# Performance work log

Measured on AMD Instinct MI355X. Metric: run time of the kernel, lower is better.

Reference implementation:

```python
import jax, jax.numpy as jnp
import numpy as np

D_MODEL = 1024
N_HEADS = 16
D_HEAD = D_MODEL // N_HEADS
LN_EPS = 1e-5


def setup_inputs() -> dict:
    key = jax.random.key(0)
    ks = jax.random.split(key, 8)
    B, T = 4, 2048
    s = 1.0 / np.sqrt(D_MODEL)
    return {
        "encoder_seq": jax.random.normal(ks[0], (B, T, D_MODEL), jnp.float32),
        "decoder_seq": jax.random.normal(ks[1], (B, T, D_MODEL), jnp.float32),
        "Wq": jax.random.normal(ks[2], (D_MODEL, D_MODEL), jnp.float32) * s,
        "bq": jnp.zeros((D_MODEL,), jnp.float32),
        "Wk": jax.random.normal(ks[3], (D_MODEL, D_MODEL), jnp.float32) * s,
        "bk": jnp.zeros((D_MODEL,), jnp.float32),
        "Wv": jax.random.normal(ks[4], (D_MODEL, D_MODEL), jnp.float32) * s,
        "bv": jnp.zeros((D_MODEL,), jnp.float32),
        "ln_gamma": jnp.ones((D_MODEL,), jnp.float32),
        "ln_beta": jnp.zeros((D_MODEL,), jnp.float32),
    }


def layer_norm(x, gamma, beta):
    mu = jnp.mean(x, axis=-1, keepdims=True)
    var = jnp.mean(jnp.square(x - mu), axis=-1, keepdims=True)
    return (x - mu) * jax.lax.rsqrt(var + LN_EPS) * gamma + beta


def reference(encoder_seq, decoder_seq, Wq, bq, Wk, bk, Wv, bv, ln_gamma, ln_beta):
    B, T_dec, _ = decoder_seq.shape
    T_enc = encoder_seq.shape[1]
    # projections (torch Linear: x @ W^T + b)
    q = (decoder_seq @ Wq.T + bq).reshape(B, T_dec, N_HEADS, D_HEAD)
    k = (encoder_seq @ Wk.T + bk).reshape(B, T_enc, N_HEADS, D_HEAD)
    v = (encoder_seq @ Wv.T + bv).reshape(B, T_enc, N_HEADS, D_HEAD)
    scale = 1.0 / np.sqrt(D_HEAD)
    # softmax-free attention: scale*(Q K^T) V == scale * Q (K^T V); avoid [T_dec,T_enc]
    kv = jnp.einsum("bthd,bthe->bhde", k, v)          # [B,H,dh,dh]
    att = jnp.einsum("bqhd,bhde->bqhe", q, kv) * scale  # [B,T_dec,H,dh]
    att = att.reshape(B, T_dec, D_MODEL)
    # dropout is identity in eval mode; residual + LayerNorm
    return layer_norm(att + decoder_seq, ln_gamma, ln_beta)
```

## Files before the change

kernel.cpp:

```cpp
#include <hip/hip_runtime.h>
#include <hip/hip_bf16.h>
#include <stdint.h>
#include <stddef.h>

typedef __attribute__((ext_vector_type(8))) __bf16 bf16x8;
typedef __attribute__((ext_vector_type(4))) float f32x4;

#define DMODEL 1024
#define HEADS  16
#define BATCH  4
#define TSEQ   2048
#define MROWS  (BATCH * TSEQ)
#define NE     (MROWS * DMODEL)
#define NW     (DMODEL * DMODEL)

#define MiB (size_t)1048576
#define QB_OFF   ((size_t)0)
#define KB_OFF   (16 * MiB)
#define VB_OFF   (32 * MiB)
#define ENC_OFF  (48 * MiB)
#define KVP_OFF  (48 * MiB)
#define DEC_OFF  (64 * MiB)
#define WB_OFF   (80 * MiB)
#define KVT_OFF  (86 * MiB)

__global__ __launch_bounds__(256)
void conv_all(const float* __restrict__ enc, const float* __restrict__ dec,
              const float* __restrict__ Wq, const float* __restrict__ Wk,
              const float* __restrict__ Wv,
              __bf16* __restrict__ encB, __bf16* __restrict__ decB,
              __bf16* __restrict__ WB)
{
    const int i = (blockIdx.x * 256 + threadIdx.x) * 8;
    const float* src;
    __bf16* dst;
    int off;
    if (i < NE)            { src = enc; dst = encB; off = i; }
    else if (i < 2 * NE)   { src = dec; dst = decB; off = i - NE; }
    else {
        const int j = i - 2 * NE;
        const int sel = j >> 20;
        off = j & (NW - 1);
        src = (sel == 0) ? Wq : (sel == 1) ? Wk : Wv;
        dst = WB + (size_t)sel * NW;
    }
    f32x4 a = *(const f32x4*)(src + off);
    f32x4 b = *(const f32x4*)(src + off + 4);
    bf16x8 o;
#pragma unroll
    for (int j = 0; j < 4; ++j) { o[j] = (__bf16)a[j]; o[j + 4] = (__bf16)b[j]; }
    *(bf16x8*)(dst + off) = o;
}

__device__ __forceinline__ bf16x8 frag(const __bf16* reg, int rowl, int kh, int g4)
{
    const int slot = ((kh << 2) + g4) ^ (rowl & 7);
    return *(const bf16x8*)(reg + rowl * 64 + slot * 8);
}

__device__ __forceinline__ void stage_half(const __bf16* gbase, int kt,
                                           __bf16* reg, int tid)
{
#pragma unroll
    for (int p = 0; p < 2; ++p) {
        const int c = tid + p * 512;
        const int row = c >> 3, slot = c & 7;
        const __bf16* src = gbase + (size_t)row * DMODEL + kt * 64
                            + ((slot ^ (row & 7)) << 3);
        __builtin_amdgcn_global_load_lds(
            (const __attribute__((address_space(1))) void*)src,
            (__attribute__((address_space(3))) void*)(reg + c * 8), 16, 0, 0);
    }
}

#define VMW(N)  asm volatile("s_waitcnt vmcnt(" #N ")" ::: "memory")
#define LGKM0() asm volatile("s_waitcnt lgkmcnt(0)" ::: "memory")

#define KPHASE(PAR, STAGE_CODE, WAIT_CODE)                                    \
  {                                                                           \
    bf16x8 af[4][2], bfv[4][2];                                               \
    _Pragma("unroll") for (int mf = 0; mf < 4; ++mf)                          \
      _Pragma("unroll") for (int kh = 0; kh < 2; ++kh)                        \
        af[mf][kh] = frag(&ldsA[(PAR) * 8192], wm * 64 + mf * 16 + l4, kh, g4); \
    _Pragma("unroll") for (int nf = 0; nf < 4; ++nf)                          \
      _Pragma("unroll") for (int kh = 0; kh < 2; ++kh)                        \
        bfv[nf][kh] = frag(&ldsB[(PAR) * 16384 + bh2 * 8192],                 \
                           (wn & 1) * 64 + nf * 16 + l4, kh, g4);             \
    LGKM0();                                                                  \
    __builtin_amdgcn_sched_barrier(0);                                        \
    __builtin_amdgcn_s_barrier();                                             \
    STAGE_CODE;                                                               \
    __builtin_amdgcn_sched_barrier(0);                                        \
    __builtin_amdgcn_s_setprio(1);                                            \
    _Pragma("unroll") for (int mf = 0; mf < 4; ++mf)                          \
      _Pragma("unroll") for (int nf = 0; nf < 4; ++nf)                        \
        _Pragma("unroll") for (int kh = 0; kh < 2; ++kh)                      \
          acc[mf][nf] = __builtin_amdgcn_mfma_f32_16x16x32_bf16(              \
              af[mf][kh], bfv[nf][kh], acc[mf][nf], 0, 0, 0);                 \
    __builtin_amdgcn_s_setprio(0);                                            \
    WAIT_CODE;                                                                \
    __builtin_amdgcn_s_barrier();                                             \
  }

__global__ __launch_bounds__(512, 2)
void qkv_gemm(const __bf16* __restrict__ decB, const __bf16* __restrict__ encB,
              const __bf16* __restrict__ WB,
              const float* __restrict__ bq, const float* __restrict__ bk,
              const float* __restrict__ bv,
              __bf16* __restrict__ Qb, __bf16* __restrict__ Kb,
              __bf16* __restrict__ Vb)
{
    __shared__ __align__(16) __bf16 ldsA[2 * 8192];
    __shared__ __align__(16) __bf16 ldsB[2 * 16384];

    const int tid  = threadIdx.x;
    const int lane = tid & 63;
    const int wv   = tid >> 6;
    const int wm   = wv >> 2;
    const int wn   = wv & 3;
    const int bh2  = wn >> 1;
    const int l4   = lane & 15;
    const int g4   = lane >> 4;

    const int bid  = blockIdx.x;
    const int slab = bid & 7;
    const int idx  = bid >> 3;
    const int r    = idx >> 3;
    const int sel  = r >> 2;
    const int bn   = r & 3;
    const int bm   = slab * 8 + (idx & 7);

    const __bf16* A    = (sel == 0) ? decB : encB;
    const __bf16* Wb   = WB + (size_t)sel * NW + (size_t)(bn * 256) * DMODEL;
    const float*  bias = (sel == 0) ? bq : (sel == 1) ? bk : bv;
    __bf16*       C    = (sel == 0) ? Qb : (sel == 1) ? Kb : Vb;

    const __bf16* Ab = A + (size_t)(bm * 128) * DMODEL;

    auto stage_tile = [&](int par, int kt) {
        stage_half(Ab,                        kt, ldsA + par * 8192,         tid);
        stage_half(Wb,                        kt, ldsB + par * 16384,        tid);
        stage_half(Wb + (size_t)128 * DMODEL, kt, ldsB + par * 16384 + 8192, tid);
    };

    f32x4 acc[4][4] = {};

    stage_tile(0, 0);
    stage_tile(1, 1);
    VMW(6);
    __builtin_amdgcn_sched_barrier(0);
    __builtin_amdgcn_s_barrier();

    for (int i = 0; i < 8; ++i) {
        KPHASE(0, { if (i < 7) stage_tile(0, 2 * i + 2); },
                  { if (i < 7) { VMW(6); } else { VMW(0); } })
        KPHASE(1, { if (i < 7) stage_tile(1, 2 * i + 3); },
                  { if (i < 7) { VMW(6); } else { VMW(0); } })
    }

#pragma unroll
    for (int mf = 0; mf < 4; ++mf)
#pragma unroll
        for (int nf = 0; nf < 4; ++nf) {
            const int gm0 = bm * 128 + wm * 64 + mf * 16 + g4 * 4;
            const int gn  = bn * 256 + wn * 64 + nf * 16 + l4;
            const float bv2 = bias[gn];
#pragma unroll
            for (int j = 0; j < 4; ++j)
                C[(size_t)(gm0 + j) * DMODEL + gn] =
                    (__bf16)(acc[mf][nf][j] + bv2);
        }
}

__global__ __launch_bounds__(256)
void kv_mm(const __bf16* __restrict__ Kb, const __bf16* __restrict__ Vb,
           float* __restrict__ kvp)
{
    __shared__ __align__(16) float Ks[128][64];
    __shared__ __align__(16) float Vs[128][64];

    const int tid = threadIdx.x;
    const int bh  = blockIdx.x;
    const int ch  = blockIdx.y;
    const int b   = bh >> 4, h = bh & 15;
    const int w   = tid >> 6, lane = tid & 63;
    const int dg  = (lane >> 3) * 8;
    const int eg  = (lane & 7) * 8;
    const size_t base = (size_t)b * TSEQ + (size_t)ch * 512;

    f32x4 acc[8][2] = {};

    for (int ss = 0; ss < 4; ++ss) {
        __syncthreads();
#pragma unroll
        for (int i = 0; i < 4; ++i) {
            const int e = i * 2048 + tid * 8;
            const int t = e >> 6, d = e & 63;
            bf16x8 k8 = *(const bf16x8*)&Kb[(base + ss * 128 + t) * DMODEL + h * 64 + d];
            bf16x8 v8 = *(const bf16x8*)&Vb[(base + ss * 128 + t) * DMODEL + h * 64 + d];
            f32x4 kf0, kf1, vf0, vf1;
#pragma unroll
            for (int j = 0; j < 4; ++j) {
                kf0[j] = (float)k8[j]; kf1[j] = (float)k8[j + 4];
                vf0[j] = (float)v8[j]; vf1[j] = (float)v8[j + 4];
            }
            *(f32x4*)&Ks[t][d]     = kf0;
            *(f32x4*)&Ks[t][d + 4] = kf1;
            *(f32x4*)&Vs[t][d]     = vf0;
            *(f32x4*)&Vs[t][d + 4] = vf1;
        }
        __syncthreads();

#pragma unroll 4
        for (int tt = 0; tt < 32; ++tt) {
            const int t = w * 32 + tt;
            f32x4 kd0 = *(const f32x4*)&Ks[t][dg];
            f32x4 kd1 = *(const f32x4*)&Ks[t][dg + 4];
            f32x4 ve0 = *(const f32x4*)&Vs[t][eg];
            f32x4 ve1 = *(const f32x4*)&Vs[t][eg + 4];
#pragma unroll
            for (int rr = 0; rr < 8; ++rr) {
                const float kd = (rr < 4) ? kd0[rr] : kd1[rr - 4];
                acc[rr][0] += ve0 * kd;
                acc[rr][1] += ve1 * kd;
            }
        }
    }

    float* red = &Ks[0][0];
    __syncthreads();
    if (w >= 2) {
        float* dstw = red + (w - 2) * 4096 + dg * 64 + eg;
#pragma unroll
        for (int rr = 0; rr < 8; ++rr) {
            *(f32x4*)(dstw + rr * 64)     = acc[rr][0];
            *(f32x4*)(dstw + rr * 64 + 4) = acc[rr][1];
        }
    }
    __syncthreads();
    if (w < 2) {
        const float* srcw = red + w * 4096 + dg * 64 + eg;
#pragma unroll
        for (int rr = 0; rr < 8; ++rr) {
            acc[rr][0] += *(const f32x4*)(srcw + rr * 64);
            acc[rr][1] += *(const f32x4*)(srcw + rr * 64 + 4);
        }
    }
    __syncthreads();
    if (w == 1) {
        float* dstw = red + dg * 64 + eg;
#pragma unroll
        for (int rr = 0; rr < 8; ++rr) {
            *(f32x4*)(dstw + rr * 64)     = acc[rr][0];
            *(f32x4*)(dstw + rr * 64 + 4) = acc[rr][1];
        }
    }
    __syncthreads();
    if (w == 0) {
        const float* srcw = red + dg * 64 + eg;
        float* o = kvp + ((size_t)ch * 64 + bh) * 4096 + (size_t)dg * 64 + eg;
#pragma unroll
        for (int rr = 0; rr < 8; ++rr) {
            f32x4 s0 = acc[rr][0] + *(const f32x4*)(srcw + rr * 64);
            f32x4 s1 = acc[rr][1] + *(const f32x4*)(srcw + rr * 64 + 4);
            *(f32x4*)(o + rr * 64)     = s0;
            *(f32x4*)(o + rr * 64 + 4) = s1;
        }
    }
}

__global__ __launch_bounds__(256)
void kv_reduce(const float* __restrict__ kvp, __bf16* __restrict__ kvT)
{
    const int idx = blockIdx.x * 256 + threadIdx.x;
    const int bh  = idx >> 12;
    const int rem = idx & 4095;
    const int d = rem >> 6, e = rem & 63;
    float s = 0.f;
#pragma unroll
    for (int c = 0; c < 4; ++c) s += kvp[((size_t)c * 64 + bh) * 4096 + rem];
    kvT[(size_t)bh * 4096 + e * 64 + d] = (__bf16)(s * 0.125f);
}

__global__ __launch_bounds__(256)
void att_ln(const __bf16* __restrict__ Q, const __bf16* __restrict__ kvT,
            const __bf16* __restrict__ decB, const float* __restrict__ gamma,
            const float* __restrict__ beta, float* __restrict__ out)
{
    __shared__ __align__(16) __bf16 att_s[32][1032];

    const int tid  = threadIdx.x;
    const int lane = tid & 63;
    const int w    = tid >> 6;
    const int l4   = lane & 15, g4 = lane >> 4;
    const int t0   = blockIdx.x * 32;
    const int b    = t0 >> 11;

#pragma unroll
    for (int i = 0; i < 4; ++i) {
        const int h = w * 4 + i;
        f32x4 acc[2][4] = {};
#pragma unroll
        for (int kk = 0; kk < 2; ++kk) {
            bf16x8 a0 = *(const bf16x8*)&Q[(size_t)(t0 + l4) * DMODEL + h * 64 + kk * 32 + g4 * 8];
            bf16x8 a1 = *(const bf16x8*)&Q[(size_t)(t0 + 16 + l4) * DMODEL + h * 64 + kk * 32 + g4 * 8];
#pragma unroll
            for (int n = 0; n < 4; ++n) {
                bf16x8 bb = *(const bf16x8*)&kvT[(size_t)(b * 16 + h) * 4096 + (n * 16 + l4) * 64 + kk * 32 + g4 * 8];
                acc[0][n] = __builtin_amdgcn_mfma_f32_16x16x32_bf16(a0, bb, acc[0][n], 0, 0, 0);
                acc[1][n] = __builtin_amdgcn_mfma_f32_16x16x32_bf16(a1, bb, acc[1][n], 0, 0, 0);
            }
        }
#pragma unroll
        for (int m = 0; m < 2; ++m)
#pragma unroll
            for (int n = 0; n < 4; ++n)
#pragma unroll
                for (int j = 0; j < 4; ++j)
                    att_s[m * 16 + g4 * 4 + j][h * 64 + n * 16 + l4] = (__bf16)acc[m][n][j];
    }
    __syncthreads();

    const int rr = tid >> 3, seg = tid & 7;
    const size_t grow = (size_t)t0 + rr;
    float sum = 0.f, ss2 = 0.f;
#pragma unroll
    for (int i = 0; i < 16; ++i) {
        const int c0 = seg * 8 + i * 64;
        bf16x8 av = *(const bf16x8*)&att_s[rr][c0];
        bf16x8 dv = *(const bf16x8*)&decB[grow * DMODEL + c0];
        bf16x8 xs;
#pragma unroll
        for (int j = 0; j < 8; ++j) {
            const float x = (float)av[j] + (float)dv[j];
            sum += x; ss2 += x * x;
            xs[j] = (__bf16)x;
        }
        *(bf16x8*)&att_s[rr][c0] = xs;
    }
    sum += __shfl_xor(sum, 1); ss2 += __shfl_xor(ss2, 1);
    sum += __shfl_xor(sum, 2); ss2 += __shfl_xor(ss2, 2);
    sum += __shfl_xor(sum, 4); ss2 += __shfl_xor(ss2, 4);
    const float mu   = sum * (1.f / 1024.f);
    const float var  = ss2 * (1.f / 1024.f) - mu * mu;
    const float rstd = rsqrtf(var + 1e-5f);

#pragma unroll
    for (int i = 0; i < 16; ++i) {
        const int c0 = seg * 8 + i * 64;
        bf16x8 xv = *(const bf16x8*)&att_s[rr][c0];
        f32x4 g0 = *(const f32x4*)&gamma[c0];
        f32x4 g1 = *(const f32x4*)&gamma[c0 + 4];
        f32x4 b0 = *(const f32x4*)&beta[c0];
        f32x4 b1 = *(const f32x4*)&beta[c0 + 4];
        f32x4 y0, y1;
#pragma unroll
        for (int j = 0; j < 4; ++j) {
            y0[j] = ((float)xv[j]     - mu) * rstd * g0[j] + b0[j];
            y1[j] = ((float)xv[j + 4] - mu) * rstd * g1[j] + b1[j];
        }
        *(f32x4*)&out[grow * DMODEL + c0]     = y0;
        *(f32x4*)&out[grow * DMODEL + c0 + 4] = y1;
    }
}

extern "C" void kernel_launch(void* const* d_in, const int* in_sizes, int n_in,
                              void* d_out, int out_size, void* d_ws, size_t ws_size,
                              hipStream_t stream)
{
    const float* enc   = (const float*)d_in[0];
    const float* dec   = (const float*)d_in[1];
    const float* Wq    = (const float*)d_in[2];
    const float* bq    = (const float*)d_in[3];
    const float* Wk    = (const float*)d_in[4];
    const float* bk    = (const float*)d_in[5];
    const float* Wv    = (const float*)d_in[6];
    const float* bv    = (const float*)d_in[7];
    const float* gamma = (const float*)d_in[8];
    const float* beta  = (const float*)d_in[9];

    char* ws = (char*)d_ws;
    __bf16* Qb   = (__bf16*)(ws + QB_OFF);
    __bf16* Kb   = (__bf16*)(ws + KB_OFF);
    __bf16* Vb   = (__bf16*)(ws + VB_OFF);
    __bf16* encB = (__bf16*)(ws + ENC_OFF);
    float*  kvp  = (float*) (ws + KVP_OFF);
    __bf16* decB = (__bf16*)(ws + DEC_OFF);
    __bf16* WB   = (__bf16*)(ws + WB_OFF);
    __bf16* kvT  = (__bf16*)(ws + KVT_OFF);

    conv_all<<<9728, 256, 0, stream>>>(enc, dec, Wq, Wk, Wv, encB, decB, WB);
    qkv_gemm<<<768, 512, 0, stream>>>(decB, encB, WB, bq, bk, bv, Qb, Kb, Vb);
    kv_mm<<<dim3(64, 4), 256, 0, stream>>>(Kb, Vb, kvp);
    kv_reduce<<<1024, 256, 0, stream>>>(kvp, kvT);
    att_ln<<<256, 256, 0, stream>>>(Qb, kvT, decB, gamma, beta, (float*)d_out);
}
```

Before: 123.4 us.

## Fuse activation fp32-to-bf16 conversion into GEMM staging, drop activation pre-conversion

```diff
diff --git a/kernel.cpp b/kernel.cpp
--- a/kernel.cpp
+++ b/kernel.cpp
@@ -18,48 +18,61 @@
 #define QB_OFF   ((size_t)0)
 #define KB_OFF   (16 * MiB)
 #define VB_OFF   (32 * MiB)
-#define ENC_OFF  (48 * MiB)
 #define KVP_OFF  (48 * MiB)
-#define DEC_OFF  (64 * MiB)
-#define WB_OFF   (80 * MiB)
-#define KVT_OFF  (86 * MiB)
+#define WB_OFF   (52 * MiB)
+#define KVT_OFF  (58 * MiB)
 
 __global__ __launch_bounds__(256)
-void conv_all(const float* __restrict__ enc, const float* __restrict__ dec,
-              const float* __restrict__ Wq, const float* __restrict__ Wk,
-              const float* __restrict__ Wv,
-              __bf16* __restrict__ encB, __bf16* __restrict__ decB,
-              __bf16* __restrict__ WB)
-{
-    const int i = (blockIdx.x * 256 + threadIdx.x) * 8;
-    const float* src;
-    __bf16* dst;
-    int off;
-    if (i < NE)            { src = enc; dst = encB; off = i; }
-    else if (i < 2 * NE)   { src = dec; dst = decB; off = i - NE; }
-    else {
-        const int j = i - 2 * NE;
-        const int sel = j >> 20;
-        off = j & (NW - 1);
-        src = (sel == 0) ? Wq : (sel == 1) ? Wk : Wv;
-        dst = WB + (size_t)sel * NW;
-    }
-    f32x4 a = *(const f32x4*)(src + off);
-    f32x4 b = *(const f32x4*)(src + off + 4);
+void conv_w(const float* __restrict__ Wq, const float* __restrict__ Wk,
+            const float* __restrict__ Wv, __bf16* __restrict__ WB)
+{
+    const int bid = blockIdx.x;
+    const int sel = bid >> 9, blk = bid & 511;
+    const float* src = (sel == 0) ? Wq : (sel == 1) ? Wk : Wv;
+    const int i = blk * 2048 + threadIdx.x * 8;
+    f32x4 a = *(const f32x4*)(src + i);
+    f32x4 b = *(const f32x4*)(src + i + 4);
     bf16x8 o;
 #pragma unroll
     for (int j = 0; j < 4; ++j) { o[j] = (__bf16)a[j]; o[j + 4] = (__bf16)b[j]; }
-    *(bf16x8*)(dst + off) = o;
-}
-
-__device__ __forceinline__ bf16x8 frag(const __bf16* reg, int rowl, int kh, int g4)
+    *(bf16x8*)&WB[(size_t)sel * NW + i] = o;
+}
+
+__device__ __forceinline__ bf16x8 fragB(const __bf16* reg, int rowl, int kh, int g4)
 {
     const int slot = ((kh << 2) + g4) ^ (rowl & 7);
     return *(const bf16x8*)(reg + rowl * 64 + slot * 8);
 }
 
-__device__ __forceinline__ void stage_half(const __bf16* gbase, int kt,
-                                           __bf16* reg, int tid)
+__device__ __forceinline__ bf16x8 fragA32(const float* buf, int rowl, int kh, int g4)
+{
+    const int s0 = kh * 8 + g4 * 2;
+    const float* base = buf + rowl * 64;
+    f32x4 a = *(const f32x4*)(base + ((s0 ^ (rowl & 15)) << 2));
+    f32x4 b = *(const f32x4*)(base + (((s0 + 1) ^ (rowl & 15)) << 2));
+    bf16x8 o;
+#pragma unroll
+    for (int j = 0; j < 4; ++j) { o[j] = (__bf16)a[j]; o[j + 4] = (__bf16)b[j]; }
+    return o;
+}
+
+__device__ __forceinline__ void stageA32(const float* gbase, int kt,
+                                         float* reg, int tid)
+{
+#pragma unroll
+    for (int p = 0; p < 4; ++p) {
+        const int c = tid + p * 512;
+        const int row = c >> 4, slot = c & 15;
+        const float* src = gbase + (size_t)row * DMODEL + kt * 64
+                           + ((slot ^ (row & 15)) << 2);
+        __builtin_amdgcn_global_load_lds(
+            (const __attribute__((address_space(1))) void*)src,
+            (__attribute__((address_space(3))) void*)(reg + c * 4), 16, 0, 0);
+    }
+}
+
+__device__ __forceinline__ void stage_halfB(const __bf16* gbase, int kt,
+                                            __bf16* reg, int tid)
 {
 #pragma unroll
     for (int p = 0; p < 2; ++p) {
@@ -81,11 +94,11 @@
     bf16x8 af[4][2], bfv[4][2];                                               \
     _Pragma("unroll") for (int mf = 0; mf < 4; ++mf)                          \
       _Pragma("unroll") for (int kh = 0; kh < 2; ++kh)                        \
-        af[mf][kh] = frag(&ldsA[(PAR) * 8192], wm * 64 + mf * 16 + l4, kh, g4); \
+        af[mf][kh] = fragA32(&ldsAf[(PAR) * 8192], wm * 64 + mf * 16 + l4, kh, g4); \
     _Pragma("unroll") for (int nf = 0; nf < 4; ++nf)                          \
       _Pragma("unroll") for (int kh = 0; kh < 2; ++kh)                        \
-        bfv[nf][kh] = frag(&ldsB[(PAR) * 16384 + bh2 * 8192],                 \
-                           (wn & 1) * 64 + nf * 16 + l4, kh, g4);             \
+        bfv[nf][kh] = fragB(&ldsB[(PAR) * 16384 + bh2 * 8192],                \
+                            (wn & 1) * 64 + nf * 16 + l4, kh, g4);            \
     LGKM0();                                                                  \
     __builtin_amdgcn_sched_barrier(0);                                        \
     __builtin_amdgcn_s_barrier();                                             \
@@ -103,14 +116,14 @@
   }
 
 __global__ __launch_bounds__(512, 2)
-void qkv_gemm(const __bf16* __restrict__ decB, const __bf16* __restrict__ encB,
+void qkv_gemm(const float* __restrict__ dec, const float* __restrict__ enc,
               const __bf16* __restrict__ WB,
               const float* __restrict__ bq, const float* __restrict__ bk,
               const float* __restrict__ bv,
               __bf16* __restrict__ Qb, __bf16* __restrict__ Kb,
               __bf16* __restrict__ Vb)
 {
-    __shared__ __align__(16) __bf16 ldsA[2 * 8192];
+    __shared__ __align__(16) float  ldsAf[2 * 8192];
     __shared__ __align__(16) __bf16 ldsB[2 * 16384];
 
     const int tid  = threadIdx.x;
@@ -130,32 +143,32 @@
     const int bn   = r & 3;
     const int bm   = slab * 8 + (idx & 7);
 
-    const __bf16* A    = (sel == 0) ? decB : encB;
+    const float*  A    = (sel == 0) ? dec : enc;
     const __bf16* Wb   = WB + (size_t)sel * NW + (size_t)(bn * 256) * DMODEL;
     const float*  bias = (sel == 0) ? bq : (sel == 1) ? bk : bv;
     __bf16*       C    = (sel == 0) ? Qb : (sel == 1) ? Kb : Vb;
 
-    const __bf16* Ab = A + (size_t)(bm * 128) * DMODEL;
+    const float* Ab = A + (size_t)(bm * 128) * DMODEL;
 
     auto stage_tile = [&](int par, int kt) {
-        stage_half(Ab,                        kt, ldsA + par * 8192,         tid);
-        stage_half(Wb,                        kt, ldsB + par * 16384,        tid);
-        stage_half(Wb + (size_t)128 * DMODEL, kt, ldsB + par * 16384 + 8192, tid);
+        stageA32(Ab, kt, ldsAf + par * 8192, tid);
+        stage_halfB(Wb,                        kt, ldsB + par * 16384,        tid);
+        stage_halfB(Wb + (size_t)128 * DMODEL, kt, ldsB + par * 16384 + 8192, tid);
     };
 
     f32x4 acc[4][4] = {};
 
     stage_tile(0, 0);
     stage_tile(1, 1);
-    VMW(6);
+    VMW(8);
     __builtin_amdgcn_sched_barrier(0);
     __builtin_amdgcn_s_barrier();
 
     for (int i = 0; i < 8; ++i) {
         KPHASE(0, { if (i < 7) stage_tile(0, 2 * i + 2); },
-                  { if (i < 7) { VMW(6); } else { VMW(0); } })
+                  { if (i < 7) { VMW(8); } else { VMW(0); } })
         KPHASE(1, { if (i < 7) stage_tile(1, 2 * i + 3); },
-                  { if (i < 7) { VMW(6); } else { VMW(0); } })
+                  { if (i < 7) { VMW(8); } else { VMW(0); } })
     }
 
 #pragma unroll
@@ -284,7 +297,7 @@
 
 __global__ __launch_bounds__(256)
 void att_ln(const __bf16* __restrict__ Q, const __bf16* __restrict__ kvT,
-            const __bf16* __restrict__ decB, const float* __restrict__ gamma,
+            const float* __restrict__ dec, const float* __restrict__ gamma,
             const float* __restrict__ beta, float* __restrict__ out)
 {
     __shared__ __align__(16) __bf16 att_s[32][1032];
@@ -328,13 +341,15 @@
     for (int i = 0; i < 16; ++i) {
         const int c0 = seg * 8 + i * 64;
         bf16x8 av = *(const bf16x8*)&att_s[rr][c0];
-        bf16x8 dv = *(const bf16x8*)&decB[grow * DMODEL + c0];
+        f32x4 d0 = *(const f32x4*)&dec[grow * DMODEL + c0];
+        f32x4 d1 = *(const f32x4*)&dec[grow * DMODEL + c0 + 4];
         bf16x8 xs;
 #pragma unroll
-        for (int j = 0; j < 8; ++j) {
-            const float x = (float)av[j] + (float)dv[j];
-            sum += x; ss2 += x * x;
-            xs[j] = (__bf16)x;
+        for (int j = 0; j < 4; ++j) {
+            const float x0 = (float)av[j] + d0[j];
+            const float x1 = (float)av[j + 4] + d1[j];
+            sum += x0 + x1; ss2 += x0 * x0 + x1 * x1;
+            xs[j] = (__bf16)x0; xs[j + 4] = (__bf16)x1;
         }
         *(bf16x8*)&att_s[rr][c0] = xs;
     }
@@ -380,18 +395,16 @@
     const float* beta  = (const float*)d_in[9];
 
     char* ws = (char*)d_ws;
-    __bf16* Qb   = (__bf16*)(ws + QB_OFF);
-    __bf16* Kb   = (__bf16*)(ws + KB_OFF);
-    __bf16* Vb   = (__bf16*)(ws + VB_OFF);
-    __bf16* encB = (__bf16*)(ws + ENC_OFF);
-    float*  kvp  = (float*) (ws + KVP_OFF);
-    __bf16* decB = (__bf16*)(ws + DEC_OFF);
-    __bf16* WB   = (__bf16*)(ws + WB_OFF);
-    __bf16* kvT  = (__bf16*)(ws + KVT_OFF);
-
-    conv_all<<<9728, 256, 0, stream>>>(enc, dec, Wq, Wk, Wv, encB, decB, WB);
-    qkv_gemm<<<768, 512, 0, stream>>>(decB, encB, WB, bq, bk, bv, Qb, Kb, Vb);
+    __bf16* Qb  = (__bf16*)(ws + QB_OFF);
+    __bf16* Kb  = (__bf16*)(ws + KB_OFF);
+    __bf16* Vb  = (__bf16*)(ws + VB_OFF);
+    float*  kvp = (float*) (ws + KVP_OFF);
+    __bf16* WB  = (__bf16*)(ws + WB_OFF);
+    __bf16* kvT = (__bf16*)(ws + KVT_OFF);
+
+    conv_w<<<1536, 256, 0, stream>>>(Wq, Wk, Wv, WB);
+    qkv_gemm<<<768, 512, 0, stream>>>(dec, enc, WB, bq, bk, bv, Qb, Kb, Vb);
     kv_mm<<<dim3(64, 4), 256, 0, stream>>>(Kb, Vb, kvp);
     kv_reduce<<<1024, 256, 0, stream>>>(kvp, kvT);
-    att_ln<<<256, 256, 0, stream>>>(Qb, kvT, decB, gamma, beta, (float*)d_out);
-}
+    att_ln<<<256, 256, 0, stream>>>(Qb, kvT, dec, gamma, beta, (float*)d_out);
+}
```

After: 129.3 us. 4.7% more time.
